# Optimization experiments

Hardware: AMD Instinct MI355X
Metric: run time of the kernel (lower is better)

The kernel has to match this reference:

```python
import jax, jax.numpy as jnp
import numpy as np

S, I, H = 4096, 2048, 2048


def setup_inputs() -> dict:
    key = jax.random.key(0)
    ks = jax.random.split(key, 7)
    k = 1.0 / np.sqrt(H)  # torch LSTMCell init range (values don't affect math shape)
    x = jax.random.normal(ks[0], (S, I), dtype=jnp.float32)
    W_ih = jax.random.uniform(ks[1], (4 * H, I), minval=-k, maxval=k, dtype=jnp.float32)
    W_hh = jax.random.uniform(ks[2], (4 * H, H), minval=-k, maxval=k, dtype=jnp.float32)
    b_ih = jax.random.uniform(ks[3], (4 * H,), minval=-k, maxval=k, dtype=jnp.float32)
    b_hh = jax.random.uniform(ks[4], (4 * H,), minval=-k, maxval=k, dtype=jnp.float32)
    xav = np.sqrt(2.0 / (1 + H))  # xavier_normal_ std for a (1, H) tensor
    h0 = jax.random.normal(ks[5], (1, H), dtype=jnp.float32) * xav
    c0 = jax.random.normal(ks[6], (1, H), dtype=jnp.float32) * xav
    return {"x": x, "W_ih": W_ih, "W_hh": W_hh, "b_ih": b_ih, "b_hh": b_hh, "h0": h0, "c0": c0}


def reference(x, W_ih, W_hh, b_ih, b_hh, h0, c0):
    # Precompute input contribution for all timesteps in one big GEMM: (S, 4H)
    x_gates = x @ W_ih.T + b_ih + b_hh
    W_hh_T = W_hh.T  # (H, 4H)

    def step(carry, xg_t):
        h, c = carry  # each (H,)
        gates = xg_t + h @ W_hh_T  # (4H,)
        i, f, g, o = jnp.split(gates, 4)
        i = jax.nn.sigmoid(i)
        f = jax.nn.sigmoid(f)
        g = jnp.tanh(g)
        o = jax.nn.sigmoid(o)
        c_new = f * c + i * g
        h_new = o * jnp.tanh(c_new)
        return (h_new, c_new), h_new

    _, hs = jax.lax.scan(step, (h0[0], c0[0]), x_gates)
    return hs[:, None, :]  # (S, 1, H) matching torch.stack of (1, H) states
```

## Files before the change

### kernel.cpp

```cpp
#include <hip/hip_runtime.h>
#include <hip/hip_bf16.h>

#define S_LEN 4096
#define IDIM  2048
#define HDIM  2048
#define G4    8192
#define NB    256
#define TPB   512
#define SENT  0x7FC00000u

typedef __attribute__((ext_vector_type(2))) float  f32x2;
typedef __attribute__((ext_vector_type(4))) float  f32x4;
typedef __attribute__((ext_vector_type(8))) short  bf16x8;

#define PKFMA(acc, w, h) \
  asm("v_pk_fma_f32 %0, %1, %2, %0" : "+v"(acc) : "v"(w), "v"(h))

__device__ __forceinline__ unsigned short f2bf(float f) {
  unsigned u = __float_as_uint(f);
  unsigned r = (u + 0x7FFFu + ((u >> 16) & 1u)) >> 16;
  return (unsigned short)r;
}
__device__ __forceinline__ float bf2f(unsigned short h) {
  return __uint_as_float(((unsigned)h) << 16);
}

__global__ __launch_bounds__(256) void fill_sentinel(unsigned long long* p) {
  const unsigned long long v =
      ((unsigned long long)SENT << 32) | (unsigned long long)SENT;
  const int n = S_LEN * HDIM / 2;
  for (int i = blockIdx.x * 256 + threadIdx.x; i < n; i += gridDim.x * 256)
    __hip_atomic_store(p + i, v, __ATOMIC_RELAXED, __HIP_MEMORY_SCOPE_AGENT);
}

#define BM 128
#define BKK 32
#define LDK 40

__global__ __launch_bounds__(256) void gemm_xg_mfma(
    const float* __restrict__ x, const float* __restrict__ Wih,
    const float* __restrict__ bih, const float* __restrict__ bhh,
    unsigned short* __restrict__ xg) {
  __shared__ unsigned short As[BM][LDK];
  __shared__ unsigned short Bs[BM][LDK];

  const int t = threadIdx.x;
  const int lane = t & 63, wid = t >> 6;
  const int wr = wid >> 1, wc = wid & 1;

  int bid = ((int)blockIdx.x & 7) * 256 + ((int)blockIdx.x >> 3);
  const int s0 = (bid >> 6) * BM;
  const int j0 = (bid & 63) * BM;

  f32x4 acc[4][4] = {};

  float bias[4];
#pragma unroll
  for (int n = 0; n < 4; ++n) {
    const int col = j0 + wc * 64 + n * 16 + (lane & 15);
    bias[n] = bih[col] + bhh[col];
  }

  for (int k0 = 0; k0 < IDIM; k0 += BKK) {
    float4 va[4], vb[4];
#pragma unroll
    for (int u = 0; u < 4; ++u) {
      const int f = t + 256 * u;
      const int row = f >> 3, kc = (f & 7) * 4;
      va[u] = *(const float4*)&x  [(size_t)(s0 + row) * IDIM + k0 + kc];
      vb[u] = *(const float4*)&Wih[(size_t)(j0 + row) * IDIM + k0 + kc];
    }
    __syncthreads();
#pragma unroll
    for (int u = 0; u < 4; ++u) {
      const int f = t + 256 * u;
      const int row = f >> 3, kc = (f & 7) * 4;
      ushort4 pa, pb;
      pa.x = f2bf(va[u].x); pa.y = f2bf(va[u].y);
      pa.z = f2bf(va[u].z); pa.w = f2bf(va[u].w);
      pb.x = f2bf(vb[u].x); pb.y = f2bf(vb[u].y);
      pb.z = f2bf(vb[u].z); pb.w = f2bf(vb[u].w);
      *(ushort4*)&As[row][kc] = pa;
      *(ushort4*)&Bs[row][kc] = pb;
    }
    __syncthreads();

    const int fr = lane & 15, koff = (lane >> 4) * 8;
    bf16x8 a[4], bfr[4];
#pragma unroll
    for (int m = 0; m < 4; ++m)
      a[m] = *(const bf16x8*)&As[wr * 64 + m * 16 + fr][koff];
#pragma unroll
    for (int n = 0; n < 4; ++n)
      bfr[n] = *(const bf16x8*)&Bs[wc * 64 + n * 16 + fr][koff];
#pragma unroll
    for (int m = 0; m < 4; ++m)
#pragma unroll
      for (int n = 0; n < 4; ++n)
        acc[m][n] = __builtin_amdgcn_mfma_f32_16x16x32_bf16(
            a[m], bfr[n], acc[m][n], 0, 0, 0);
  }

#pragma unroll
  for (int m = 0; m < 4; ++m) {
    const int row0 = s0 + wr * 64 + m * 16 + (lane >> 4) * 4;
#pragma unroll
    for (int n = 0; n < 4; ++n) {
      const int col = j0 + wc * 64 + n * 16 + (lane & 15);
#pragma unroll
      for (int r = 0; r < 4; ++r)
        xg[(size_t)(row0 + r) * G4 + col] = f2bf(acc[m][n][r] + bias[n]);
    }
  }
}

__global__ __launch_bounds__(TPB, 2) void lstm_scan(
    const unsigned short* __restrict__ xg, const float* __restrict__ Whh,
    const float* __restrict__ h0, const float* __restrict__ c0,
    float* __restrict__ out) {
  __shared__ __align__(16) float h_sh[HDIM];

  const int b = blockIdx.x, t = threadIdx.x;
  const int lane = t & 63, wid = t >> 6;
  const int j = b * 8 + wid;

  f32x2 w2[4][16];
#pragma unroll
  for (int g = 0; g < 4; ++g) {
    const float* wp = Whh + ((size_t)g * HDIM + j) * HDIM + lane * 4;
#pragma unroll
    for (int i = 0; i < 8; ++i) {
      const float4 v = *(const float4*)(wp + i * 256);
      w2[g][i * 2 + 0] = f32x2{v.x, v.y};
      w2[g][i * 2 + 1] = f32x2{v.z, v.w};
    }
  }
  float c_reg = (lane == 0) ? c0[j] : 0.f;

  for (int ts = 0; ts < S_LEN; ++ts) {
    float xgv = 0.f;
    if (lane < 4)
      xgv = bf2f(xg[(size_t)ts * G4 + (size_t)lane * HDIM + j]);

    if (ts == 0) {
      h_sh[2*t]        = h0[2*t];
      h_sh[2*t + 1]    = h0[2*t + 1];
      h_sh[2*t + 1024] = h0[2*t + 1024];
      h_sh[2*t + 1025] = h0[2*t + 1025];
    } else {
      const unsigned long long* src =
          (const unsigned long long*)(out + (size_t)(ts - 1) * HDIM);
      unsigned long long r0 = 0, r1 = 0;
      int d0 = 0, d1 = 0;
      for (;;) {
        if (!d0) {
          r0 = __hip_atomic_load(src + t, __ATOMIC_RELAXED,
                                 __HIP_MEMORY_SCOPE_AGENT);
          d0 = ((unsigned)r0 != SENT) & ((unsigned)(r0 >> 32) != SENT);
        }
        if (!d1) {
          r1 = __hip_atomic_load(src + t + 512, __ATOMIC_RELAXED,
                                 __HIP_MEMORY_SCOPE_AGENT);
          d1 = ((unsigned)r1 != SENT) & ((unsigned)(r1 >> 32) != SENT);
        }
        if (d0 & d1) break;
        __builtin_amdgcn_s_sleep(1);
      }
      h_sh[2*t]        = __uint_as_float((unsigned)r0);
      h_sh[2*t + 1]    = __uint_as_float((unsigned)(r0 >> 32));
      h_sh[2*t + 1024] = __uint_as_float((unsigned)r1);
      h_sh[2*t + 1025] = __uint_as_float((unsigned)(r1 >> 32));
    }
    __syncthreads();

    f32x2 A0 = {0.f, 0.f}, A1 = {0.f, 0.f}, A2 = {0.f, 0.f}, A3 = {0.f, 0.f};
    const f32x4* h4 = (const f32x4*)&h_sh[lane * 4];
#pragma unroll
    for (int i = 0; i < 8; ++i) {
      const f32x4 hv = h4[i * 64];
      const f32x2 hlo = {hv.x, hv.y}, hhi = {hv.z, hv.w};
      PKFMA(A0, w2[0][i*2+0], hlo); PKFMA(A0, w2[0][i*2+1], hhi);
      PKFMA(A1, w2[1][i*2+0], hlo); PKFMA(A1, w2[1][i*2+1], hhi);
      PKFMA(A2, w2[2][i*2+0], hlo); PKFMA(A2, w2[2][i*2+1], hhi);
      PKFMA(A3, w2[3][i*2+0], hlo); PKFMA(A3, w2[3][i*2+1], hhi);
    }
    float a0 = A0.x + A0.y, a1 = A1.x + A1.y;
    float a2 = A2.x + A2.y, a3 = A3.x + A3.y;
#pragma unroll
    for (int m = 1; m < 64; m <<= 1) {
      a0 += __shfl_xor(a0, m);
      a1 += __shfl_xor(a1, m);
      a2 += __shfl_xor(a2, m);
      a3 += __shfl_xor(a3, m);
    }
    float sv = (lane == 0) ? a0 : (lane == 1) ? a1 : (lane == 2) ? a2 : a3;
    sv += xgv;
    const float av = (lane == 2) ? tanhf(sv) : 1.f / (1.f + __expf(-sv));
    const float iv = __shfl(av, 0);
    const float fv = __shfl(av, 1);
    const float gv = __shfl(av, 2);
    const float ov = __shfl(av, 3);
    if (lane == 0) {
      c_reg = fmaf(fv, c_reg, iv * gv);
      const float hn = ov * tanhf(c_reg);
      __hip_atomic_store(&out[(size_t)ts * HDIM + j], hn,
                         __ATOMIC_RELAXED, __HIP_MEMORY_SCOPE_AGENT);
    }
  }
}

extern "C" void kernel_launch(void* const* d_in, const int* in_sizes, int n_in,
                              void* d_out, int out_size, void* d_ws, size_t ws_size,
                              hipStream_t stream) {
  const float* x   = (const float*)d_in[0];
  const float* Wih = (const float*)d_in[1];
  const float* Whh = (const float*)d_in[2];
  const float* bih = (const float*)d_in[3];
  const float* bhh = (const float*)d_in[4];
  const float* h0  = (const float*)d_in[5];
  const float* c0  = (const float*)d_in[6];
  float* out = (float*)d_out;

  unsigned short* xg = (unsigned short*)d_ws;

  fill_sentinel<<<dim3(2048), 256, 0, stream>>>((unsigned long long*)out);
  gemm_xg_mfma<<<dim3(2048), 256, 0, stream>>>(x, Wih, bih, bhh, xg);
  void* args[] = {(void*)&xg, (void*)&Whh, (void*)&h0, (void*)&c0, (void*)&out};
  hipLaunchCooperativeKernel((void*)lstm_scan, dim3(NB), dim3(TPB),
                             args, 0, stream);
}
```

Measured before the change: 14.00 ms.

## Add per-block step flags to gate cross-block h polling; use fast activations

Adds a per-block progress flag array. Wave 0 of each block polls the 256 flags before the block reads the previous hidden state, instead of every thread spinning on sentinel values across all of h. Sigmoid and tanh now use rcp-based approximations, and the sentinel fill uses plain stores. This aims to cut polling traffic on the scan's critical path. It adds an extra barrier and a flag store per step, and the sentinel re-check is kept as a fallback for memory ordering.

```diff
diff --git a/kernel.cpp b/kernel.cpp
--- a/kernel.cpp
+++ b/kernel.cpp
@@ -24,13 +24,19 @@
 __device__ __forceinline__ float bf2f(unsigned short h) {
   return __uint_as_float(((unsigned)h) << 16);
 }
+__device__ __forceinline__ float sigmoid_fast(float x) {
+  return __builtin_amdgcn_rcpf(1.f + __expf(-x));
+}
+__device__ __forceinline__ float tanh_fast(float x) {
+  return 1.f - 2.f * __builtin_amdgcn_rcpf(__expf(2.f * x) + 1.f);
+}
 
 __global__ __launch_bounds__(256) void fill_sentinel(unsigned long long* p) {
   const unsigned long long v =
       ((unsigned long long)SENT << 32) | (unsigned long long)SENT;
   const int n = S_LEN * HDIM / 2;
   for (int i = blockIdx.x * 256 + threadIdx.x; i < n; i += gridDim.x * 256)
-    __hip_atomic_store(p + i, v, __ATOMIC_RELAXED, __HIP_MEMORY_SCOPE_AGENT);
+    p[i] = v;
 }
 
 #define BM 128
@@ -117,7 +123,7 @@
 __global__ __launch_bounds__(TPB, 2) void lstm_scan(
     const unsigned short* __restrict__ xg, const float* __restrict__ Whh,
     const float* __restrict__ h0, const float* __restrict__ c0,
-    float* __restrict__ out) {
+    float* __restrict__ out, unsigned* __restrict__ flags) {
   __shared__ __align__(16) float h_sh[HDIM];
 
   const int b = blockIdx.x, t = threadIdx.x;
@@ -143,29 +149,36 @@
       xgv = bf2f(xg[(size_t)ts * G4 + (size_t)lane * HDIM + j]);
 
     if (ts == 0) {
+      __syncthreads();
       h_sh[2*t]        = h0[2*t];
       h_sh[2*t + 1]    = h0[2*t + 1];
       h_sh[2*t + 1024] = h0[2*t + 1024];
       h_sh[2*t + 1025] = h0[2*t + 1025];
     } else {
+      if (wid == 0) {
+        const unsigned want = (unsigned)ts;
+        unsigned f0 = 0, f1 = 0, f2 = 0, f3 = 0;
+        for (;;) {
+          if (f0 < want) f0 = __hip_atomic_load(&flags[lane],       __ATOMIC_RELAXED, __HIP_MEMORY_SCOPE_AGENT);
+          if (f1 < want) f1 = __hip_atomic_load(&flags[lane +  64], __ATOMIC_RELAXED, __HIP_MEMORY_SCOPE_AGENT);
+          if (f2 < want) f2 = __hip_atomic_load(&flags[lane + 128], __ATOMIC_RELAXED, __HIP_MEMORY_SCOPE_AGENT);
+          if (f3 < want) f3 = __hip_atomic_load(&flags[lane + 192], __ATOMIC_RELAXED, __HIP_MEMORY_SCOPE_AGENT);
+          if (f0 >= want && f1 >= want && f2 >= want && f3 >= want) break;
+          __builtin_amdgcn_s_sleep(1);
+        }
+      }
+      __syncthreads();
       const unsigned long long* src =
           (const unsigned long long*)(out + (size_t)(ts - 1) * HDIM);
-      unsigned long long r0 = 0, r1 = 0;
-      int d0 = 0, d1 = 0;
-      for (;;) {
-        if (!d0) {
-          r0 = __hip_atomic_load(src + t, __ATOMIC_RELAXED,
-                                 __HIP_MEMORY_SCOPE_AGENT);
-          d0 = ((unsigned)r0 != SENT) & ((unsigned)(r0 >> 32) != SENT);
-        }
-        if (!d1) {
-          r1 = __hip_atomic_load(src + t + 512, __ATOMIC_RELAXED,
-                                 __HIP_MEMORY_SCOPE_AGENT);
-          d1 = ((unsigned)r1 != SENT) & ((unsigned)(r1 >> 32) != SENT);
-        }
-        if (d0 & d1) break;
-        __builtin_amdgcn_s_sleep(1);
-      }
+      unsigned long long r0, r1;
+      do {
+        r0 = __hip_atomic_load(src + t, __ATOMIC_RELAXED,
+                               __HIP_MEMORY_SCOPE_AGENT);
+      } while (((unsigned)r0 == SENT) | ((unsigned)(r0 >> 32) == SENT));
+      do {
+        r1 = __hip_atomic_load(src + t + 512, __ATOMIC_RELAXED,
+                               __HIP_MEMORY_SCOPE_AGENT);
+      } while (((unsigned)r1 == SENT) | ((unsigned)(r1 >> 32) == SENT));
       h_sh[2*t]        = __uint_as_float((unsigned)r0);
       h_sh[2*t + 1]    = __uint_as_float((unsigned)(r0 >> 32));
       h_sh[2*t + 1024] = __uint_as_float((unsigned)r1);
@@ -195,17 +208,23 @@
     }
     float sv = (lane == 0) ? a0 : (lane == 1) ? a1 : (lane == 2) ? a2 : a3;
     sv += xgv;
-    const float av = (lane == 2) ? tanhf(sv) : 1.f / (1.f + __expf(-sv));
+    const float av = (lane == 2) ? tanh_fast(sv) : sigmoid_fast(sv);
     const float iv = __shfl(av, 0);
     const float fv = __shfl(av, 1);
     const float gv = __shfl(av, 2);
     const float ov = __shfl(av, 3);
     if (lane == 0) {
       c_reg = fmaf(fv, c_reg, iv * gv);
-      const float hn = ov * tanhf(c_reg);
+      const float hn = ov * tanh_fast(c_reg);
       __hip_atomic_store(&out[(size_t)ts * HDIM + j], hn,
                          __ATOMIC_RELAXED, __HIP_MEMORY_SCOPE_AGENT);
     }
+    asm volatile("" ::: "memory");
+    __builtin_amdgcn_s_barrier();
+    asm volatile("" ::: "memory");
+    if (t == 0)
+      __hip_atomic_store(&flags[b], (unsigned)(ts + 1),
+                         __ATOMIC_RELAXED, __HIP_MEMORY_SCOPE_AGENT);
   }
 }
 
@@ -221,11 +240,16 @@
   const float* c0  = (const float*)d_in[6];
   float* out = (float*)d_out;
 
-  unsigned short* xg = (unsigned short*)d_ws;
+  unsigned* flags = (unsigned*)d_ws;
+  unsigned short* xg = (unsigned short*)((char*)d_ws + 32768);
+
+  hipMemsetAsync(flags, 0, NB * sizeof(unsigned), stream);
 
   fill_sentinel<<<dim3(2048), 256, 0, stream>>>((unsigned long long*)out);
   gemm_xg_mfma<<<dim3(2048), 256, 0, stream>>>(x, Wih, bih, bhh, xg);
-  void* args[] = {(void*)&xg, (void*)&Whh, (void*)&h0, (void*)&c0, (void*)&out};
+
+  void* args[] = {(void*)&xg, (void*)&Whh, (void*)&h0,
+                  (void*)&c0, (void*)&out, (void*)&flags};
   hipLaunchCooperativeKernel((void*)lstm_scan, dim3(NB), dim3(TPB),
                              args, 0, stream);
 }
```

Result: faster. 12.23 ms (-12.7%).

## Poll hidden state with one wavefront per block and forward own outputs locally

Applied to the files above, without the earlier changes.

Cross-block synchronisation in the recurrent scan is restructured. Each block gathers its 8 outputs in shared memory and wavefront 0 stores them. The same wavefront then polls the global h vector for the next step, skips its own entries, and stages the rest into shared memory, instead of all 512 threads polling. Weights move into named scalar registers under launch bounds with one block per SM, and sigmoid/tanh now use reciprocal-based fast approximations. The gain should come from less polling traffic and fewer atomic stores; the cost is an extra block barrier per step, a serialised poll on one wavefront, and slightly lower activation accuracy.

```diff
diff --git a/kernel.cpp b/kernel.cpp
--- a/kernel.cpp
+++ b/kernel.cpp
@@ -24,13 +24,19 @@
 __device__ __forceinline__ float bf2f(unsigned short h) {
   return __uint_as_float(((unsigned)h) << 16);
 }
+__device__ __forceinline__ float sigmoid_fast(float x) {
+  return __builtin_amdgcn_rcpf(1.f + __expf(-x));
+}
+__device__ __forceinline__ float tanh_fast(float x) {
+  return 1.f - 2.f * __builtin_amdgcn_rcpf(__expf(2.f * x) + 1.f);
+}
 
 __global__ __launch_bounds__(256) void fill_sentinel(unsigned long long* p) {
   const unsigned long long v =
       ((unsigned long long)SENT << 32) | (unsigned long long)SENT;
   const int n = S_LEN * HDIM / 2;
   for (int i = blockIdx.x * 256 + threadIdx.x; i < n; i += gridDim.x * 256)
-    __hip_atomic_store(p + i, v, __ATOMIC_RELAXED, __HIP_MEMORY_SCOPE_AGENT);
+    p[i] = v;
 }
 
 #define BM 128
@@ -114,76 +120,80 @@
   }
 }
 
-__global__ __launch_bounds__(TPB, 2) void lstm_scan(
+
+#define WDECL(g) f32x2 w##g##_0, w##g##_1, w##g##_2, w##g##_3, w##g##_4, \
+  w##g##_5, w##g##_6, w##g##_7, w##g##_8, w##g##_9, w##g##_10, w##g##_11, \
+  w##g##_12, w##g##_13, w##g##_14, w##g##_15;
+
+#define WLOAD(g) do { \
+  const float* wp = Whh + ((size_t)g * HDIM + j) * HDIM + lane * 4; \
+  float4 q; \
+  q = *(const float4*)(wp + 0*256); w##g##_0  = f32x2{q.x,q.y}; w##g##_1  = f32x2{q.z,q.w}; \
+  q = *(const float4*)(wp + 1*256); w##g##_2  = f32x2{q.x,q.y}; w##g##_3  = f32x2{q.z,q.w}; \
+  q = *(const float4*)(wp + 2*256); w##g##_4  = f32x2{q.x,q.y}; w##g##_5  = f32x2{q.z,q.w}; \
+  q = *(const float4*)(wp + 3*256); w##g##_6  = f32x2{q.x,q.y}; w##g##_7  = f32x2{q.z,q.w}; \
+  q = *(const float4*)(wp + 4*256); w##g##_8  = f32x2{q.x,q.y}; w##g##_9  = f32x2{q.z,q.w}; \
+  q = *(const float4*)(wp + 5*256); w##g##_10 = f32x2{q.x,q.y}; w##g##_11 = f32x2{q.z,q.w}; \
+  q = *(const float4*)(wp + 6*256); w##g##_12 = f32x2{q.x,q.y}; w##g##_13 = f32x2{q.z,q.w}; \
+  q = *(const float4*)(wp + 7*256); w##g##_14 = f32x2{q.x,q.y}; w##g##_15 = f32x2{q.z,q.w}; \
+} while (0)
+
+#define DOTI(idx, p, q_) do { \
+  const f32x4 hv = h4[idx * 64]; \
+  const f32x2 hlo = {hv.x, hv.y}, hhi = {hv.z, hv.w}; \
+  PKFMA(A0, w0_##p, hlo); PKFMA(A0, w0_##q_, hhi); \
+  PKFMA(A1, w1_##p, hlo); PKFMA(A1, w1_##q_, hhi); \
+  PKFMA(A2, w2_##p, hlo); PKFMA(A2, w2_##q_, hhi); \
+  PKFMA(A3, w3_##p, hlo); PKFMA(A3, w3_##q_, hhi); \
+} while (0)
+
+#define POLL1(i) do { if (!(dn & (1u << i))) { \
+  unsigned long long r = __hip_atomic_load(src + i * 64 + lane, \
+      __ATOMIC_RELAXED, __HIP_MEMORY_SCOPE_AGENT); \
+  if (((unsigned)r != SENT) & ((unsigned)(r >> 32) != SENT)) { \
+    v##i = r; dn |= 1u << i; } } } while (0)
+
+#define STAGE1(i) do { if (!(dn_init & (1u << i))) hq[i * 64 + lane] = v##i; } while (0)
+
+__global__ __launch_bounds__(TPB, 1) void lstm_scan(
     const unsigned short* __restrict__ xg, const float* __restrict__ Whh,
     const float* __restrict__ h0, const float* __restrict__ c0,
     float* __restrict__ out) {
   __shared__ __align__(16) float h_sh[HDIM];
+  __shared__ float h_out[8];
 
   const int b = blockIdx.x, t = threadIdx.x;
   const int lane = t & 63, wid = t >> 6;
   const int j = b * 8 + wid;
 
-  f32x2 w2[4][16];
-#pragma unroll
-  for (int g = 0; g < 4; ++g) {
-    const float* wp = Whh + ((size_t)g * HDIM + j) * HDIM + lane * 4;
-#pragma unroll
-    for (int i = 0; i < 8; ++i) {
-      const float4 v = *(const float4*)(wp + i * 256);
-      w2[g][i * 2 + 0] = f32x2{v.x, v.y};
-      w2[g][i * 2 + 1] = f32x2{v.z, v.w};
-    }
-  }
+  WDECL(0) WDECL(1) WDECL(2) WDECL(3)
+  WLOAD(0); WLOAD(1); WLOAD(2); WLOAD(3);
+
   float c_reg = (lane == 0) ? c0[j] : 0.f;
+  const f32x4* h4 = (const f32x4*)&h_sh[lane * 4];
+  unsigned long long* hq = (unsigned long long*)h_sh;
+
+  unsigned dn_init = 0;
+#pragma unroll
+  for (int i = 0; i < 16; ++i)
+    if (i * 64 + lane >= b * 4 && i * 64 + lane < b * 4 + 4)
+      dn_init |= 1u << i;
+
+  h_sh[t]        = h0[t];
+  h_sh[t + 512]  = h0[t + 512];
+  h_sh[t + 1024] = h0[t + 1024];
+  h_sh[t + 1536] = h0[t + 1536];
+  __syncthreads();
 
   for (int ts = 0; ts < S_LEN; ++ts) {
     float xgv = 0.f;
     if (lane < 4)
       xgv = bf2f(xg[(size_t)ts * G4 + (size_t)lane * HDIM + j]);
 
-    if (ts == 0) {
-      h_sh[2*t]        = h0[2*t];
-      h_sh[2*t + 1]    = h0[2*t + 1];
-      h_sh[2*t + 1024] = h0[2*t + 1024];
-      h_sh[2*t + 1025] = h0[2*t + 1025];
-    } else {
-      const unsigned long long* src =
-          (const unsigned long long*)(out + (size_t)(ts - 1) * HDIM);
-      unsigned long long r0 = 0, r1 = 0;
-      int d0 = 0, d1 = 0;
-      for (;;) {
-        if (!d0) {
-          r0 = __hip_atomic_load(src + t, __ATOMIC_RELAXED,
-                                 __HIP_MEMORY_SCOPE_AGENT);
-          d0 = ((unsigned)r0 != SENT) & ((unsigned)(r0 >> 32) != SENT);
-        }
-        if (!d1) {
-          r1 = __hip_atomic_load(src + t + 512, __ATOMIC_RELAXED,
-                                 __HIP_MEMORY_SCOPE_AGENT);
-          d1 = ((unsigned)r1 != SENT) & ((unsigned)(r1 >> 32) != SENT);
-        }
-        if (d0 & d1) break;
-        __builtin_amdgcn_s_sleep(1);
-      }
-      h_sh[2*t]        = __uint_as_float((unsigned)r0);
-      h_sh[2*t + 1]    = __uint_as_float((unsigned)(r0 >> 32));
-      h_sh[2*t + 1024] = __uint_as_float((unsigned)r1);
-      h_sh[2*t + 1025] = __uint_as_float((unsigned)(r1 >> 32));
-    }
-    __syncthreads();
-
     f32x2 A0 = {0.f, 0.f}, A1 = {0.f, 0.f}, A2 = {0.f, 0.f}, A3 = {0.f, 0.f};
-    const f32x4* h4 = (const f32x4*)&h_sh[lane * 4];
-#pragma unroll
-    for (int i = 0; i < 8; ++i) {
-      const f32x4 hv = h4[i * 64];
-      const f32x2 hlo = {hv.x, hv.y}, hhi = {hv.z, hv.w};
-      PKFMA(A0, w2[0][i*2+0], hlo); PKFMA(A0, w2[0][i*2+1], hhi);
-      PKFMA(A1, w2[1][i*2+0], hlo); PKFMA(A1, w2[1][i*2+1], hhi);
-      PKFMA(A2, w2[2][i*2+0], hlo); PKFMA(A2, w2[2][i*2+1], hhi);
-      PKFMA(A3, w2[3][i*2+0], hlo); PKFMA(A3, w2[3][i*2+1], hhi);
-    }
+    DOTI(0, 0, 1);   DOTI(1, 2, 3);   DOTI(2, 4, 5);   DOTI(3, 6, 7);
+    DOTI(4, 8, 9);   DOTI(5, 10, 11); DOTI(6, 12, 13); DOTI(7, 14, 15);
+
     float a0 = A0.x + A0.y, a1 = A1.x + A1.y;
     float a2 = A2.x + A2.y, a3 = A3.x + A3.y;
 #pragma unroll
@@ -195,17 +205,43 @@
     }
     float sv = (lane == 0) ? a0 : (lane == 1) ? a1 : (lane == 2) ? a2 : a3;
     sv += xgv;
-    const float av = (lane == 2) ? tanhf(sv) : 1.f / (1.f + __expf(-sv));
+    const float av = (lane == 2) ? tanh_fast(sv) : sigmoid_fast(sv);
     const float iv = __shfl(av, 0);
     const float fv = __shfl(av, 1);
     const float gv = __shfl(av, 2);
     const float ov = __shfl(av, 3);
     if (lane == 0) {
       c_reg = fmaf(fv, c_reg, iv * gv);
-      const float hn = ov * tanhf(c_reg);
-      __hip_atomic_store(&out[(size_t)ts * HDIM + j], hn,
-                         __ATOMIC_RELAXED, __HIP_MEMORY_SCOPE_AGENT);
-    }
+      h_out[wid] = ov * tanh_fast(c_reg);
+    }
+    __syncthreads();
+
+    if (wid == 0) {
+      if (lane < 8)
+        __hip_atomic_store(&out[(size_t)ts * HDIM + b * 8 + lane], h_out[lane],
+                           __ATOMIC_RELAXED, __HIP_MEMORY_SCOPE_AGENT);
+      if (ts + 1 < S_LEN) {
+        if (lane < 8) h_sh[b * 8 + lane] = h_out[lane];
+        const unsigned long long* src =
+            (const unsigned long long*)(out + (size_t)ts * HDIM);
+        unsigned long long v0, v1, v2, v3, v4, v5, v6, v7,
+                           v8, v9, v10, v11, v12, v13, v14, v15;
+        unsigned dn = dn_init;
+        for (;;) {
+          POLL1(0);  POLL1(1);  POLL1(2);  POLL1(3);
+          POLL1(4);  POLL1(5);  POLL1(6);  POLL1(7);
+          POLL1(8);  POLL1(9);  POLL1(10); POLL1(11);
+          POLL1(12); POLL1(13); POLL1(14); POLL1(15);
+          if (__all(dn == 0xFFFFu)) break;
+          __builtin_amdgcn_s_sleep(2);
+        }
+        STAGE1(0);  STAGE1(1);  STAGE1(2);  STAGE1(3);
+        STAGE1(4);  STAGE1(5);  STAGE1(6);  STAGE1(7);
+        STAGE1(8);  STAGE1(9);  STAGE1(10); STAGE1(11);
+        STAGE1(12); STAGE1(13); STAGE1(14); STAGE1(15);
+      }
+    }
+    __syncthreads();
   }
 }
 
@@ -225,6 +261,7 @@
 
   fill_sentinel<<<dim3(2048), 256, 0, stream>>>((unsigned long long*)out);
   gemm_xg_mfma<<<dim3(2048), 256, 0, stream>>>(x, Wih, bih, bhh, xg);
+
   void* args[] = {(void*)&xg, (void*)&Whh, (void*)&h0, (void*)&c0, (void*)&out};
   hipLaunchCooperativeKernel((void*)lstm_scan, dim3(NB), dim3(TPB),
                              args, 0, stream);
```

After: 30.48 ms. 2.18x slower.
